# Optimization experiments

Measured on AMD Instinct MI355X. Metric: run time of the kernel, lower is better.

## Reference

```python
import jax, jax.numpy as jnp
import numpy as np

N_HEADS = 16
EPS = 1e-5  # torch nn.LayerNorm default


def layernorm(x, g, b):
    mu = x.mean(-1, keepdims=True)
    var = ((x - mu) ** 2).mean(-1, keepdims=True)
    return (x - mu) * jax.lax.rsqrt(var + EPS) * g + b


def setup_inputs() -> dict:
    V, D, Dff, L, S, B = 32000, 1024, 4096, 6, 2048, 1
    key = jax.random.key(0)
    ks = jax.random.split(key, 12)
    std = 0.02  # GPT-2 init
    nrm = lambda k, shp: jax.random.normal(k, shp, jnp.float32) * std
    return {
        "tokens": jax.random.randint(ks[0], (B, S), 0, V),
        "tok_emb": nrm(ks[1], (V, D)),          # tied with lm head
        "pos_emb": nrm(ks[2], (S, D)),
        "Wq": nrm(ks[3], (L, D, D)), "bq": jnp.zeros((L, D)),
        "Wk": nrm(ks[4], (L, D, D)), "bk": jnp.zeros((L, D)),
        "Wv": nrm(ks[5], (L, D, D)), "bv": jnp.zeros((L, D)),
        "Wo": nrm(ks[6], (L, D, D)), "bo": jnp.zeros((L, D)),
        "ln1_g": jnp.ones((L, D)), "ln1_b": jnp.zeros((L, D)),
        "ln2_g": jnp.ones((L, D)), "ln2_b": jnp.zeros((L, D)),
        "W1": nrm(ks[7], (L, D, Dff)), "b1": jnp.zeros((L, Dff)),
        "W2": nrm(ks[8], (L, Dff, D)), "b2": jnp.zeros((L, D)),
        "lnf_g": jnp.ones((D,)), "lnf_b": jnp.zeros((D,)),
    }


def reference(tokens, tok_emb, pos_emb, Wq, bq, Wk, bk, Wv, bv, Wo, bo,
              ln1_g, ln1_b, ln2_g, ln2_b, W1, b1, W2, b2, lnf_g, lnf_b):
    B, S = tokens.shape
    D = tok_emb.shape[1]
    dk = D // N_HEADS
    scale = 1.0 / np.sqrt(dk)

    x = tok_emb[tokens] + pos_emb[:S][None]           # (B,S,D); dropout p=0 -> identity
    causal = jnp.tril(jnp.ones((S, S), bool))

    def block(x, p):
        wq, bq_, wk, bk_, wv, bv_, wo, bo_, g1, b1_, g2, b2_, w1, bf1, w2, bf2 = p
        # --- attention sublayer (pre-norm) ---
        h = layernorm(x, g1, b1_)
        q = (h @ wq + bq_).reshape(B, S, N_HEADS, dk)
        k = (h @ wk + bk_).reshape(B, S, N_HEADS, dk)
        v = (h @ wv + bv_).reshape(B, S, N_HEADS, dk)
        scores = jnp.einsum('bqhd,bkhd->bhqk', q, k) * scale
        scores = jnp.where(causal, scores, -jnp.inf)   # masked_fill(mask==0, -inf)
        attn = jax.nn.softmax(scores, axis=-1)
        ctx = jnp.einsum('bhqk,bkhd->bqhd', attn, v).reshape(B, S, D)
        x = x + ctx @ wo + bo_
        # --- FFN sublayer (pre-norm) ---
        h = layernorm(x, g2, b2_)
        x = x + jax.nn.gelu(h @ w1 + bf1, approximate=False) @ w2 + bf2
        return x, None

    x, _ = jax.lax.scan(
        block, x,
        (Wq, bq, Wk, bk, Wv, bv, Wo, bo, ln1_g, ln1_b, ln2_g, ln2_b, W1, b1, W2, b2))
    x = layernorm(x, lnf_g, lnf_b)
    logits = x @ tok_emb.T                             # tied lm head (no bias)
    return logits
```

## Files before the change

kernel.cpp:

```cpp
#include <hip/hip_runtime.h>
#include <hip/hip_bf16.h>
#include <cstdint>
#include <cstddef>


typedef __attribute__((ext_vector_type(4))) float  f32x4;
typedef __attribute__((ext_vector_type(8))) __bf16 bf16x8;
typedef __attribute__((ext_vector_type(4))) __bf16 bf16x4;

#define S_LEN 2048
#define DMODEL 1024
#define DFF 4096
#define NLAYER 6
#define NHEAD 16
#define DK 64
#define VOCAB 32000
#define MN (S_LEN * DMODEL)

__device__ __forceinline__ void gload_lds16(const void* g, void* l) {
    __builtin_amdgcn_global_load_lds(
        (__attribute__((address_space(1))) void*)(void*)(g),
        (__attribute__((address_space(3))) void*)(l), 16, 0, 0);
}

__global__ __launch_bounds__(256) void transpose_cvt64(
    const float* __restrict__ in, __bf16* __restrict__ out,
    int K, int N, size_t in_lstride, size_t out_lstride) {
    __shared__ float tile[64][65];
    const float* inp = in + blockIdx.z * in_lstride;
    __bf16* outp = out + blockIdx.z * out_lstride;
    const int n0 = blockIdx.x * 64, k0 = blockIdx.y * 64;
    const int t = threadIdx.x;
    const int lc = t & 15, rr = t >> 4;
#pragma unroll
    for (int i = 0; i < 4; ++i) {
        float4 v = *(const float4*)&inp[(size_t)(k0 + rr + i * 16) * N + n0 + lc * 4];
        tile[rr + i * 16][lc * 4 + 0] = v.x;
        tile[rr + i * 16][lc * 4 + 1] = v.y;
        tile[rr + i * 16][lc * 4 + 2] = v.z;
        tile[rr + i * 16][lc * 4 + 3] = v.w;
    }
    __syncthreads();
    const int a = t & 7, b = t >> 3;
#pragma unroll
    for (int j = 0; j < 2; ++j) {
        const int n = b + j * 32;
        bf16x8 o;
#pragma unroll
        for (int e = 0; e < 8; ++e) o[e] = (__bf16)tile[a * 8 + e][n];
        *(bf16x8*)&outp[(size_t)(n0 + n) * K + k0 + a * 8] = o;
    }
}

__global__ __launch_bounds__(256) void cvt_bf16(
    const float* __restrict__ in, __bf16* __restrict__ out, long n4) {
    long i = (long)blockIdx.x * 256 + threadIdx.x;
    if (i >= n4) return;
    float4 v = ((const float4*)in)[i];
    bf16x4 o = {(__bf16)v.x, (__bf16)v.y, (__bf16)v.z, (__bf16)v.w};
    ((bf16x4*)out)[i] = o;
}

__global__ __launch_bounds__(256) void embed_kernel(
    const int* __restrict__ tokens, const float* __restrict__ te,
    const float* __restrict__ pe, float* __restrict__ x) {
    const int s = blockIdx.x, t = threadIdx.x;
    const int tok = tokens[s];
    float4 a = ((const float4*)(te + (size_t)tok * DMODEL))[t];
    float4 p = ((const float4*)(pe + (size_t)s * DMODEL))[t];
    float4 r = {a.x + p.x, a.y + p.y, a.z + p.z, a.w + p.w};
    ((float4*)(x + (size_t)s * DMODEL))[t] = r;
}

template <int NPART>
__global__ __launch_bounds__(256) void ln_kernel(
    float* __restrict__ x, const float* __restrict__ p,
    const float* __restrict__ g, const float* __restrict__ b,
    __bf16* __restrict__ out) {
    const int row = blockIdx.x, t = threadIdx.x;
    float4 v = ((const float4*)(x + (size_t)row * DMODEL))[t];
    if (NPART == 2) {
        float4 a0 = ((const float4*)(p + (size_t)row * DMODEL))[t];
        float4 a1 = ((const float4*)(p + MN + (size_t)row * DMODEL))[t];
        v.x += a0.x + a1.x;
        v.y += a0.y + a1.y;
        v.z += a0.z + a1.z;
        v.w += a0.w + a1.w;
        ((float4*)(x + (size_t)row * DMODEL))[t] = v;
    }
    float s  = v.x + v.y + v.z + v.w;
    float s2 = v.x * v.x + v.y * v.y + v.z * v.z + v.w * v.w;
#pragma unroll
    for (int off = 1; off < 64; off <<= 1) {
        s  += __shfl_xor(s, off);
        s2 += __shfl_xor(s2, off);
    }
    __shared__ float ss[4], ss2[4];
    const int wave = t >> 6;
    if ((t & 63) == 0) { ss[wave] = s; ss2[wave] = s2; }
    __syncthreads();
    s  = ss[0] + ss[1] + ss[2] + ss[3];
    s2 = ss2[0] + ss2[1] + ss2[2] + ss2[3];
    const float mu  = s * (1.0f / DMODEL);
    const float var = s2 * (1.0f / DMODEL) - mu * mu;
    const float rstd = rsqrtf(var + 1e-5f);
    float4 gg = ((const float4*)g)[t];
    float4 bb = ((const float4*)b)[t];
    __bf16* o = out + (size_t)row * DMODEL + t * 4;
    o[0] = (__bf16)((v.x - mu) * rstd * gg.x + bb.x);
    o[1] = (__bf16)((v.y - mu) * rstd * gg.y + bb.y);
    o[2] = (__bf16)((v.z - mu) * rstd * gg.z + bb.z);
    o[3] = (__bf16)((v.w - mu) * rstd * gg.w + bb.w);
}

template <int BM, int BN, int BK, int SPLITK, int MODE, int XCD>
__global__ __launch_bounds__(256) void gemm_tiled(
    const __bf16* __restrict__ A, const __bf16* __restrict__ BT,
    int M, int N, int K,
    const float* __restrict__ bias,
    float* __restrict__ fout,
    __bf16* __restrict__ bfout,
    __bf16* __restrict__ qb, __bf16* __restrict__ kb, __bf16* __restrict__ vb,
    const float* __restrict__ bq, const float* __restrict__ bk,
    const float* __restrict__ bv) {
    constexpr int SLOTS = BK / 8;
    constexpr int SH    = (BK == 64) ? 0 : 1;
    constexpr int RPC   = 2048 / BK;
    constexpr int ACH_A = BM / RPC;
    constexpr int ACH_B = BN / RPC;
    constexpr int LOADS = ACH_A + ACH_B;
    constexpr int MR = BM / 32;
    constexpr int NR = BN / 32;
    constexpr int KS = BK / 32;
    __shared__ alignas(16) __bf16 As[2][BM * BK];
    __shared__ alignas(16) __bf16 Bs[2][BN * BK];
    const int t = threadIdx.x;
    const int wave = t >> 6, lane = t & 63;
    const int wr = wave >> 1, wc = wave & 1;
    const int lg = lane >> 4, lr = lane & 15;

    int bx = blockIdx.x, by = blockIdx.y;
    if (XCD) {
        const int nwg = gridDim.x * gridDim.y;
        const int wgid = by * gridDim.x + bx;
        const int sw = (wgid & 7) * (nwg >> 3) + (wgid >> 3);
        bx = sw % gridDim.x;
        by = sw / gridDim.x;
    }
    const int row0 = bx * BM, col0 = by * BN;
    const int kz = (SPLITK > 1) ? blockIdx.z : 0;
    const int Ksl = K / SPLITK;

    f32x4 acc[MR][NR];
#pragma unroll
    for (int i = 0; i < MR; i++)
#pragma unroll
        for (int j = 0; j < NR; j++) acc[i][j] = f32x4{0.f, 0.f, 0.f, 0.f};

    const int srow = t / SLOTS;
    const int sks = ((t % SLOTS) ^ ((srow >> SH) & (SLOTS - 1))) * 8;
    const __bf16* Ab = A + (size_t)(row0 + srow) * K + kz * Ksl + sks;
    const __bf16* Bb = BT + (size_t)(col0 + srow) * K + kz * Ksl + sks;

    const int nt = Ksl / BK;
#pragma unroll
    for (int ch = 0; ch < ACH_A; ++ch)
        gload_lds16(Ab + (size_t)ch * RPC * K, &As[0][ch * 2048 + wave * 512]);
#pragma unroll
    for (int ch = 0; ch < ACH_B; ++ch)
        gload_lds16(Bb + (size_t)ch * RPC * K, &Bs[0][ch * 2048 + wave * 512]);

    int c = 0;
    for (int T = 0; T < nt; ++T) {
        if (T + 1 < nt) {
            const int k0 = (T + 1) * BK;
#pragma unroll
            for (int ch = 0; ch < ACH_A; ++ch)
                gload_lds16(Ab + (size_t)ch * RPC * K + k0,
                            &As[c ^ 1][ch * 2048 + wave * 512]);
#pragma unroll
            for (int ch = 0; ch < ACH_B; ++ch)
                gload_lds16(Bb + (size_t)ch * RPC * K + k0,
                            &Bs[c ^ 1][ch * 2048 + wave * 512]);
            if constexpr (LOADS == 3)
                asm volatile("s_waitcnt vmcnt(3)" ::: "memory");
            else if constexpr (LOADS == 4)
                asm volatile("s_waitcnt vmcnt(4)" ::: "memory");
            else if constexpr (LOADS == 6)
                asm volatile("s_waitcnt vmcnt(6)" ::: "memory");
            else
                asm volatile("s_waitcnt vmcnt(8)" ::: "memory");
        } else {
            asm volatile("s_waitcnt vmcnt(0)" ::: "memory");
        }
        __builtin_amdgcn_s_barrier();
        asm volatile("" ::: "memory");

        bf16x8 af[MR][KS], bfr[NR][KS];
#pragma unroll
        for (int i = 0; i < MR; i++)
#pragma unroll
            for (int ks = 0; ks < KS; ks++) {
                const int row = wr * (BM / 2) + i * 16 + lr;
                const int ph = ((ks * 4 + lg) ^ ((row >> SH) & (SLOTS - 1)));
                af[i][ks] = *(const bf16x8*)&As[c][row * BK + ph * 8];
            }
#pragma unroll
        for (int j = 0; j < NR; j++)
#pragma unroll
            for (int ks = 0; ks < KS; ks++) {
                const int n = wc * (BN / 2) + j * 16 + lr;
                const int ph = ((ks * 4 + lg) ^ ((n >> SH) & (SLOTS - 1)));
                bfr[j][ks] = *(const bf16x8*)&Bs[c][n * BK + ph * 8];
            }
        __builtin_amdgcn_s_setprio(1);
#pragma unroll
        for (int i = 0; i < MR; i++)
#pragma unroll
            for (int j = 0; j < NR; j++)
#pragma unroll
                for (int ks = 0; ks < KS; ks++)
                    acc[i][j] = __builtin_amdgcn_mfma_f32_16x16x32_bf16(
                        af[i][ks], bfr[j][ks], acc[i][j], 0, 0, 0);
        __builtin_amdgcn_s_setprio(0);
        asm volatile("" ::: "memory");
        __builtin_amdgcn_s_barrier();
        c ^= 1;
    }

#pragma unroll
    for (int i = 0; i < MR; i++) {
#pragma unroll
        for (int j = 0; j < NR; j++) {
#pragma unroll
            for (int r = 0; r < 4; r++) {
                const int row = row0 + wr * (BM / 2) + i * 16 + lg * 4 + r;
                const int col = col0 + wc * (BN / 2) + j * 16 + lr;
                float v = acc[i][j][r];
                if (MODE == 0) {
                    const int sec = col >> 10, cn = col & 1023;
                    const int head = cn >> 6, d = cn & 63;
                    if (sec == 0) {
                        v = (v + bq[cn]) * 0.18033688011112042f;
                        qb[((size_t)head * S_LEN + row) * DK + d] = (__bf16)v;
                    } else if (sec == 1) {
                        v = v + bk[cn];
                        kb[((size_t)head * S_LEN + row) * DK + d] = (__bf16)v;
                    } else {
                        v = v + bv[cn];
                        vb[((size_t)head * DK + d) * S_LEN + row] = (__bf16)v;
                    }
                } else if (MODE == 2) {
                    const float gg = v + bias[col];
                    const float cgl = 0.5f * gg * (1.0f + erff(gg * 0.70710678118654752f));
                    bfout[(size_t)row * N + col] = (__bf16)cgl;
                } else if (MODE == 6) {
                    const float vv = v + (kz == 0 ? bias[col] : 0.f);
                    __builtin_nontemporal_store(
                        vv, &fout[(size_t)kz * MN + (size_t)row * N + col]);
                } else {
                    __builtin_nontemporal_store(v, &fout[(size_t)row * N + col]);
                }
            }
        }
    }
}

__global__ __launch_bounds__(256) void attn_kernel(
    const __bf16* __restrict__ q, const __bf16* __restrict__ k,
    const __bf16* __restrict__ vt, __bf16* __restrict__ ctx) {
    const int xb = blockIdx.x, head = blockIdx.y;
    const int t = threadIdx.x;
    const int wave = t >> 6, lane = t & 63;
    const int lg = lane >> 4, lr = lane & 15;
    const int rg = (wave < 2) ? (2 * xb + wave) : (127 - 2 * xb - (3 - wave));
    const int rowbase = rg * 16;
    const int tend = rg >> 2;

    const __bf16* qh = q + (size_t)head * S_LEN * DK;
    const __bf16* kh = k + (size_t)head * S_LEN * DK;
    const __bf16* vh = vt + (size_t)head * DK * S_LEN;

    __shared__ alignas(16) __bf16 pls[4][16 * 72];
    __bf16* pw = pls[wave];

    bf16x8 qf0 = *(const bf16x8*)&qh[(size_t)(rowbase + lr) * DK + lg * 8];
    bf16x8 qf1 = *(const bf16x8*)&qh[(size_t)(rowbase + lr) * DK + 32 + lg * 8];

    f32x4 oacc[4];
#pragma unroll
    for (int j = 0; j < 4; j++) oacc[j] = f32x4{0.f, 0.f, 0.f, 0.f};
    float m[4], l[4];
#pragma unroll
    for (int r = 0; r < 4; r++) { m[r] = -__builtin_inff(); l[r] = 0.f; }

    for (int tt = 0; tt <= tend; ++tt) {
        const int kv0 = tt * 64;
        f32x4 sc[4];
        __builtin_amdgcn_s_setprio(1);
#pragma unroll
        for (int jn = 0; jn < 4; jn++) {
            bf16x8 kf0 = *(const bf16x8*)&kh[(size_t)(kv0 + jn * 16 + lr) * DK + lg * 8];
            bf16x8 kf1 = *(const bf16x8*)&kh[(size_t)(kv0 + jn * 16 + lr) * DK + 32 + lg * 8];
            sc[jn] = __builtin_amdgcn_mfma_f32_16x16x32_bf16(
                qf0, kf0, f32x4{0.f, 0.f, 0.f, 0.f}, 0, 0, 0);
            sc[jn] = __builtin_amdgcn_mfma_f32_16x16x32_bf16(qf1, kf1, sc[jn], 0, 0, 0);
        }
        __builtin_amdgcn_s_setprio(0);

        if (tt == tend) {
#pragma unroll
            for (int jn = 0; jn < 4; jn++)
#pragma unroll
                for (int r = 0; r < 4; r++) {
                    const int qrow = rowbase + lg * 4 + r;
                    if (kv0 + jn * 16 + lr > qrow) sc[jn][r] = -__builtin_inff();
                }
        }

        float mt[4];
#pragma unroll
        for (int r = 0; r < 4; r++)
            mt[r] = fmaxf(fmaxf(sc[0][r], sc[1][r]), fmaxf(sc[2][r], sc[3][r]));
#pragma unroll
        for (int off = 1; off < 16; off <<= 1)
#pragma unroll
            for (int r = 0; r < 4; r++) mt[r] = fmaxf(mt[r], __shfl_xor(mt[r], off));

        float alpha[4], psum[4];
#pragma unroll
        for (int r = 0; r < 4; r++) {
            const float mn = fmaxf(m[r], mt[r]);
            alpha[r] = exp2f(m[r] - mn);
            m[r] = mn;
#pragma unroll
            for (int jn = 0; jn < 4; jn++) sc[jn][r] = exp2f(sc[jn][r] - mn);
            psum[r] = (sc[0][r] + sc[1][r]) + (sc[2][r] + sc[3][r]);
        }
#pragma unroll
        for (int off = 1; off < 16; off <<= 1)
#pragma unroll
            for (int r = 0; r < 4; r++) psum[r] += __shfl_xor(psum[r], off);
#pragma unroll
        for (int r = 0; r < 4; r++) l[r] = l[r] * alpha[r] + psum[r];
#pragma unroll
        for (int j = 0; j < 4; j++)
#pragma unroll
            for (int r = 0; r < 4; r++) oacc[j][r] *= alpha[r];

#pragma unroll
        for (int r = 0; r < 4; r++)
#pragma unroll
            for (int jn = 0; jn < 4; jn++)
                pw[(lg * 4 + r) * 72 + jn * 16 + lr] = (__bf16)sc[jn][r];

        bf16x8 pf0 = *(const bf16x8*)&pw[lr * 72 + lg * 8];
        bf16x8 pf1 = *(const bf16x8*)&pw[lr * 72 + 32 + lg * 8];
        __builtin_amdgcn_s_setprio(1);
#pragma unroll
        for (int j = 0; j < 4; j++) {
            bf16x8 vf0 = *(const bf16x8*)&vh[(size_t)(j * 16 + lr) * S_LEN + kv0 + lg * 8];
            oacc[j] = __builtin_amdgcn_mfma_f32_16x16x32_bf16(pf0, vf0, oacc[j], 0, 0, 0);
            bf16x8 vf1 = *(const bf16x8*)&vh[(size_t)(j * 16 + lr) * S_LEN + kv0 + 32 + lg * 8];
            oacc[j] = __builtin_amdgcn_mfma_f32_16x16x32_bf16(pf1, vf1, oacc[j], 0, 0, 0);
        }
        __builtin_amdgcn_s_setprio(0);
    }

#pragma unroll
    for (int j = 0; j < 4; j++)
#pragma unroll
        for (int r = 0; r < 4; r++) {
            const int row = rowbase + lg * 4 + r;
            ctx[(size_t)row * DMODEL + head * DK + j * 16 + lr] =
                (__bf16)(oacc[j][r] / l[r]);
        }
}

extern "C" void kernel_launch(void* const* d_in, const int* in_sizes, int n_in,
                              void* d_out, int out_size, void* d_ws, size_t ws_size,
                              hipStream_t stream) {
    const int*   tokens  = (const int*)d_in[0];
    const float* tok_emb = (const float*)d_in[1];
    const float* pos_emb = (const float*)d_in[2];
    const float* Wq = (const float*)d_in[3];
    const float* bq = (const float*)d_in[4];
    const float* Wk = (const float*)d_in[5];
    const float* bk = (const float*)d_in[6];
    const float* Wv = (const float*)d_in[7];
    const float* bv = (const float*)d_in[8];
    const float* Wo = (const float*)d_in[9];
    const float* bo = (const float*)d_in[10];
    const float* ln1_g = (const float*)d_in[11];
    const float* ln1_b = (const float*)d_in[12];
    const float* ln2_g = (const float*)d_in[13];
    const float* ln2_b = (const float*)d_in[14];
    const float* W1 = (const float*)d_in[15];
    const float* b1 = (const float*)d_in[16];
    const float* W2 = (const float*)d_in[17];
    const float* b2 = (const float*)d_in[18];
    const float* lnf_g = (const float*)d_in[19];
    const float* lnf_b = (const float*)d_in[20];

    char* ws = (char*)d_ws;
    size_t off = 0;
    auto alloc = [&](size_t bytes) {
        char* p = ws + off;
        off = (off + bytes + 255) & ~(size_t)255;
        return p;
    };
    __bf16* wqkv_t = (__bf16*)alloc((size_t)NLAYER * 3072 * 1024 * 2);
    __bf16* wo_t   = (__bf16*)alloc((size_t)NLAYER * 1024 * 1024 * 2);
    __bf16* w1_t   = (__bf16*)alloc((size_t)NLAYER * 4096 * 1024 * 2);
    __bf16* w2_t   = (__bf16*)alloc((size_t)NLAYER * 1024 * 4096 * 2);
    __bf16* temb   = (__bf16*)alloc((size_t)VOCAB * DMODEL * 2);
    float*  x      = (float*)alloc((size_t)MN * 4);
    __bf16* h      = (__bf16*)alloc((size_t)MN * 2);
    __bf16* qbuf   = (__bf16*)alloc((size_t)MN * 2);
    __bf16* kbuf   = (__bf16*)alloc((size_t)MN * 2);
    __bf16* vbuf   = (__bf16*)alloc((size_t)MN * 2);
    __bf16* ctx    = (__bf16*)alloc((size_t)MN * 2);
    __bf16* ffn    = (__bf16*)alloc((size_t)S_LEN * DFF * 2);
    if (off > ws_size) return;

    float* pproj  = (float*)ffn;
    float* pffn2  = (float*)qbuf;

    const dim3 blk256(256);

    transpose_cvt64<<<dim3(16, 16, NLAYER), blk256, 0, stream>>>(
        Wq, wqkv_t + (size_t)0 * 1024 * 1024, 1024, 1024,
        (size_t)1024 * 1024, (size_t)3072 * 1024);
    transpose_cvt64<<<dim3(16, 16, NLAYER), blk256, 0, stream>>>(
        Wk, wqkv_t + (size_t)1 * 1024 * 1024, 1024, 1024,
        (size_t)1024 * 1024, (size_t)3072 * 1024);
    transpose_cvt64<<<dim3(16, 16, NLAYER), blk256, 0, stream>>>(
        Wv, wqkv_t + (size_t)2 * 1024 * 1024, 1024, 1024,
        (size_t)1024 * 1024, (size_t)3072 * 1024);
    transpose_cvt64<<<dim3(16, 16, NLAYER), blk256, 0, stream>>>(
        Wo, wo_t, 1024, 1024, (size_t)1024 * 1024, (size_t)1024 * 1024);
    transpose_cvt64<<<dim3(64, 16, NLAYER), blk256, 0, stream>>>(
        W1, w1_t, 1024, 4096, (size_t)1024 * 4096, (size_t)4096 * 1024);
    transpose_cvt64<<<dim3(16, 64, NLAYER), blk256, 0, stream>>>(
        W2, w2_t, 4096, 1024, (size_t)4096 * 1024, (size_t)1024 * 4096);
    cvt_bf16<<<dim3((VOCAB * DMODEL / 4 + 255) / 256), blk256, 0, stream>>>(
        tok_emb, temb, (long)VOCAB * DMODEL / 4);

    embed_kernel<<<dim3(S_LEN), blk256, 0, stream>>>(tokens, tok_emb, pos_emb, x);
    ln_kernel<0><<<dim3(S_LEN), blk256, 0, stream>>>(
        x, nullptr, ln1_g, ln1_b, h);

    for (int l = 0; l < NLAYER; ++l) {
        gemm_tiled<64, 128, 64, 1, 0, 0><<<dim3(32, 24), blk256, 0, stream>>>(
            h, wqkv_t + (size_t)l * 3072 * 1024, S_LEN, 3072, 1024,
            nullptr, nullptr, nullptr, qbuf, kbuf, vbuf,
            bq + l * 1024, bk + l * 1024, bv + l * 1024);
        attn_kernel<<<dim3(32, NHEAD), blk256, 0, stream>>>(
            qbuf, kbuf, vbuf, ctx);
        gemm_tiled<64, 128, 64, 2, 6, 0><<<dim3(32, 8, 2), blk256, 0, stream>>>(
            ctx, wo_t + (size_t)l * 1024 * 1024, S_LEN, 1024, 1024,
            bo + l * 1024, pproj, nullptr, nullptr, nullptr, nullptr,
            nullptr, nullptr, nullptr);
        ln_kernel<2><<<dim3(S_LEN), blk256, 0, stream>>>(
            x, pproj, ln2_g + l * 1024, ln2_b + l * 1024, h);
        gemm_tiled<128, 128, 64, 1, 2, 0><<<dim3(16, 32), blk256, 0, stream>>>(
            h, w1_t + (size_t)l * 4096 * 1024, S_LEN, 4096, 1024,
            b1 + l * 4096, nullptr, ffn, nullptr, nullptr, nullptr,
            nullptr, nullptr, nullptr);
        gemm_tiled<64, 128, 64, 2, 6, 0><<<dim3(32, 8, 2), blk256, 0, stream>>>(
            ffn, w2_t + (size_t)l * 1024 * 4096, S_LEN, 1024, 4096,
            b2 + l * 1024, pffn2, nullptr, nullptr, nullptr, nullptr,
            nullptr, nullptr, nullptr);
        if (l + 1 < NLAYER) {
            ln_kernel<2><<<dim3(S_LEN), blk256, 0, stream>>>(
                x, pffn2, ln1_g + (l + 1) * 1024, ln1_b + (l + 1) * 1024, h);
        }
    }

    ln_kernel<2><<<dim3(S_LEN), blk256, 0, stream>>>(x, pffn2, lnf_g, lnf_b, h);
    gemm_tiled<128, 256, 32, 1, 3, 1><<<dim3(16, 125), blk256, 0, stream>>>(
        h, temb, S_LEN, VOCAB, 1024,
        nullptr, (float*)d_out, nullptr, nullptr, nullptr, nullptr,
        nullptr, nullptr, nullptr);
}
```

Before: 1.717 ms.

## Widen attention KV tile, merge QKVO transposes, fuse embed into LayerNorm, retile QKV GEMM

The attention kernel now processes 128 keys per iteration instead of 64, which halves the loop trips and softmax reductions but needs more registers and a larger LDS P buffer. The four Q/K/V/O weight transposes become one launch, and the embedding lookup is folded into the first LayerNorm kernel, removing launches and one round trip of x through memory. The QKV projection GEMM switches to 128-row tiles, which gives fewer, larger blocks. The wider attention tile also makes causal-diagonal handling coarser, so some fully masked work is wasted.

```diff
diff --git a/kernel.cpp b/kernel.cpp
--- a/kernel.cpp
+++ b/kernel.cpp
@@ -23,14 +23,10 @@
         (__attribute__((address_space(3))) void*)(l), 16, 0, 0);
 }
 
-__global__ __launch_bounds__(256) void transpose_cvt64(
-    const float* __restrict__ in, __bf16* __restrict__ out,
-    int K, int N, size_t in_lstride, size_t out_lstride) {
+__device__ __forceinline__ void tr64_body(
+    const float* __restrict__ inp, __bf16* __restrict__ outp,
+    int K, int N, int n0, int k0, int t) {
     __shared__ float tile[64][65];
-    const float* inp = in + blockIdx.z * in_lstride;
-    __bf16* outp = out + blockIdx.z * out_lstride;
-    const int n0 = blockIdx.x * 64, k0 = blockIdx.y * 64;
-    const int t = threadIdx.x;
     const int lc = t & 15, rr = t >> 4;
 #pragma unroll
     for (int i = 0; i < 4; ++i) {
@@ -50,6 +46,27 @@
         for (int e = 0; e < 8; ++e) o[e] = (__bf16)tile[a * 8 + e][n];
         *(bf16x8*)&outp[(size_t)(n0 + n) * K + k0 + a * 8] = o;
     }
+}
+
+__global__ __launch_bounds__(256) void transpose_cvt64(
+    const float* __restrict__ in, __bf16* __restrict__ out,
+    int K, int N, size_t in_lstride, size_t out_lstride) {
+    tr64_body(in + blockIdx.z * in_lstride, out + blockIdx.z * out_lstride,
+              K, N, blockIdx.x * 64, blockIdx.y * 64, threadIdx.x);
+}
+
+__global__ __launch_bounds__(256) void transpose_qkvo(
+    const float* __restrict__ Wq, const float* __restrict__ Wk,
+    const float* __restrict__ Wv, const float* __restrict__ Wo,
+    __bf16* __restrict__ wqkv_t, __bf16* __restrict__ wo_t) {
+    const int z = blockIdx.z, mat = z & 3, l = z >> 2;
+    const float* src =
+        (mat == 0 ? Wq : mat == 1 ? Wk : mat == 2 ? Wv : Wo) +
+        (size_t)l * 1024 * 1024;
+    __bf16* dst = (mat < 3)
+        ? wqkv_t + (size_t)l * 3072 * 1024 + (size_t)mat * 1024 * 1024
+        : wo_t + (size_t)l * 1024 * 1024;
+    tr64_body(src, dst, 1024, 1024, blockIdx.x * 64, blockIdx.y * 64, threadIdx.x);
 }
 
 __global__ __launch_bounds__(256) void cvt_bf16(
@@ -61,24 +78,24 @@
     ((bf16x4*)out)[i] = o;
 }
 
-__global__ __launch_bounds__(256) void embed_kernel(
-    const int* __restrict__ tokens, const float* __restrict__ te,
-    const float* __restrict__ pe, float* __restrict__ x) {
-    const int s = blockIdx.x, t = threadIdx.x;
-    const int tok = tokens[s];
-    float4 a = ((const float4*)(te + (size_t)tok * DMODEL))[t];
-    float4 p = ((const float4*)(pe + (size_t)s * DMODEL))[t];
-    float4 r = {a.x + p.x, a.y + p.y, a.z + p.z, a.w + p.w};
-    ((float4*)(x + (size_t)s * DMODEL))[t] = r;
-}
-
-template <int NPART>
+template <int NPART, int EMBED>
 __global__ __launch_bounds__(256) void ln_kernel(
     float* __restrict__ x, const float* __restrict__ p,
     const float* __restrict__ g, const float* __restrict__ b,
-    __bf16* __restrict__ out) {
+    __bf16* __restrict__ out,
+    const int* __restrict__ tokens, const float* __restrict__ te,
+    const float* __restrict__ pe) {
     const int row = blockIdx.x, t = threadIdx.x;
-    float4 v = ((const float4*)(x + (size_t)row * DMODEL))[t];
+    float4 v;
+    if (EMBED) {
+        const int tok = tokens[row];
+        float4 a = ((const float4*)(te + (size_t)tok * DMODEL))[t];
+        float4 q = ((const float4*)(pe + (size_t)row * DMODEL))[t];
+        v = float4{a.x + q.x, a.y + q.y, a.z + q.z, a.w + q.w};
+        ((float4*)(x + (size_t)row * DMODEL))[t] = v;
+    } else {
+        v = ((const float4*)(x + (size_t)row * DMODEL))[t];
+    }
     if (NPART == 2) {
         float4 a0 = ((const float4*)(p + (size_t)row * DMODEL))[t];
         float4 a1 = ((const float4*)(p + MN + (size_t)row * DMODEL))[t];
@@ -275,13 +292,13 @@
     const int lg = lane >> 4, lr = lane & 15;
     const int rg = (wave < 2) ? (2 * xb + wave) : (127 - 2 * xb - (3 - wave));
     const int rowbase = rg * 16;
-    const int tend = rg >> 2;
+    const int tend = rg >> 3;
 
     const __bf16* qh = q + (size_t)head * S_LEN * DK;
     const __bf16* kh = k + (size_t)head * S_LEN * DK;
     const __bf16* vh = vt + (size_t)head * DK * S_LEN;
 
-    __shared__ alignas(16) __bf16 pls[4][16 * 72];
+    __shared__ alignas(16) __bf16 pls[4][16 * 136];
     __bf16* pw = pls[wave];
 
     bf16x8 qf0 = *(const bf16x8*)&qh[(size_t)(rowbase + lr) * DK + lg * 8];
@@ -295,11 +312,11 @@
     for (int r = 0; r < 4; r++) { m[r] = -__builtin_inff(); l[r] = 0.f; }
 
     for (int tt = 0; tt <= tend; ++tt) {
-        const int kv0 = tt * 64;
-        f32x4 sc[4];
+        const int kv0 = tt * 128;
+        f32x4 sc[8];
         __builtin_amdgcn_s_setprio(1);
 #pragma unroll
-        for (int jn = 0; jn < 4; jn++) {
+        for (int jn = 0; jn < 8; jn++) {
             bf16x8 kf0 = *(const bf16x8*)&kh[(size_t)(kv0 + jn * 16 + lr) * DK + lg * 8];
             bf16x8 kf1 = *(const bf16x8*)&kh[(size_t)(kv0 + jn * 16 + lr) * DK + 32 + lg * 8];
             sc[jn] = __builtin_amdgcn_mfma_f32_16x16x32_bf16(
@@ -310,7 +327,7 @@
 
         if (tt == tend) {
 #pragma unroll
-            for (int jn = 0; jn < 4; jn++)
+            for (int jn = 0; jn < 8; jn++)
 #pragma unroll
                 for (int r = 0; r < 4; r++) {
                     const int qrow = rowbase + lg * 4 + r;
@@ -320,8 +337,11 @@
 
         float mt[4];
 #pragma unroll
-        for (int r = 0; r < 4; r++)
-            mt[r] = fmaxf(fmaxf(sc[0][r], sc[1][r]), fmaxf(sc[2][r], sc[3][r]));
+        for (int r = 0; r < 4; r++) {
+            float a0 = fmaxf(fmaxf(sc[0][r], sc[1][r]), fmaxf(sc[2][r], sc[3][r]));
+            float a1 = fmaxf(fmaxf(sc[4][r], sc[5][r]), fmaxf(sc[6][r], sc[7][r]));
+            mt[r] = fmaxf(a0, a1);
+        }
 #pragma unroll
         for (int off = 1; off < 16; off <<= 1)
 #pragma unroll
@@ -334,8 +354,9 @@
             alpha[r] = exp2f(m[r] - mn);
             m[r] = mn;
 #pragma unroll
-            for (int jn = 0; jn < 4; jn++) sc[jn][r] = exp2f(sc[jn][r] - mn);
-            psum[r] = (sc[0][r] + sc[1][r]) + (sc[2][r] + sc[3][r]);
+            for (int jn = 0; jn < 8; jn++) sc[jn][r] = exp2f(sc[jn][r] - mn);
+            psum[r] = ((sc[0][r] + sc[1][r]) + (sc[2][r] + sc[3][r])) +
+                      ((sc[4][r] + sc[5][r]) + (sc[6][r] + sc[7][r]));
         }
 #pragma unroll
         for (int off = 1; off < 16; off <<= 1)
@@ -351,18 +372,23 @@
 #pragma unroll
         for (int r = 0; r < 4; r++)
 #pragma unroll
-            for (int jn = 0; jn < 4; jn++)
-                pw[(lg * 4 + r) * 72 + jn * 16 + lr] = (__bf16)sc[jn][r];
-
-        bf16x8 pf0 = *(const bf16x8*)&pw[lr * 72 + lg * 8];
-        bf16x8 pf1 = *(const bf16x8*)&pw[lr * 72 + 32 + lg * 8];
+            for (int jn = 0; jn < 8; jn++)
+                pw[(lg * 4 + r) * 136 + jn * 16 + lr] = (__bf16)sc[jn][r];
+
+        bf16x8 pf[4];
+#pragma unroll
+        for (int h = 0; h < 4; h++)
+            pf[h] = *(const bf16x8*)&pw[lr * 136 + h * 32 + lg * 8];
         __builtin_amdgcn_s_setprio(1);
 #pragma unroll
         for (int j = 0; j < 4; j++) {
-            bf16x8 vf0 = *(const bf16x8*)&vh[(size_t)(j * 16 + lr) * S_LEN + kv0 + lg * 8];
-            oacc[j] = __builtin_amdgcn_mfma_f32_16x16x32_bf16(pf0, vf0, oacc[j], 0, 0, 0);
-            bf16x8 vf1 = *(const bf16x8*)&vh[(size_t)(j * 16 + lr) * S_LEN + kv0 + 32 + lg * 8];
-            oacc[j] = __builtin_amdgcn_mfma_f32_16x16x32_bf16(pf1, vf1, oacc[j], 0, 0, 0);
+#pragma unroll
+            for (int h = 0; h < 4; h++) {
+                bf16x8 vf = *(const bf16x8*)
+                    &vh[(size_t)(j * 16 + lr) * S_LEN + kv0 + h * 32 + lg * 8];
+                oacc[j] = __builtin_amdgcn_mfma_f32_16x16x32_bf16(
+                    pf[h], vf, oacc[j], 0, 0, 0);
+            }
         }
         __builtin_amdgcn_s_setprio(0);
     }
@@ -428,17 +454,8 @@
 
     const dim3 blk256(256);
 
-    transpose_cvt64<<<dim3(16, 16, NLAYER), blk256, 0, stream>>>(
-        Wq, wqkv_t + (size_t)0 * 1024 * 1024, 1024, 1024,
-        (size_t)1024 * 1024, (size_t)3072 * 1024);
-    transpose_cvt64<<<dim3(16, 16, NLAYER), blk256, 0, stream>>>(
-        Wk, wqkv_t + (size_t)1 * 1024 * 1024, 1024, 1024,
-        (size_t)1024 * 1024, (size_t)3072 * 1024);
-    transpose_cvt64<<<dim3(16, 16, NLAYER), blk256, 0, stream>>>(
-        Wv, wqkv_t + (size_t)2 * 1024 * 1024, 1024, 1024,
-        (size_t)1024 * 1024, (size_t)3072 * 1024);
-    transpose_cvt64<<<dim3(16, 16, NLAYER), blk256, 0, stream>>>(
-        Wo, wo_t, 1024, 1024, (size_t)1024 * 1024, (size_t)1024 * 1024);
+    transpose_qkvo<<<dim3(16, 16, 4 * NLAYER), blk256, 0, stream>>>(
+        Wq, Wk, Wv, Wo, wqkv_t, wo_t);
     transpose_cvt64<<<dim3(64, 16, NLAYER), blk256, 0, stream>>>(
         W1, w1_t, 1024, 4096, (size_t)1024 * 4096, (size_t)4096 * 1024);
     transpose_cvt64<<<dim3(16, 64, NLAYER), blk256, 0, stream>>>(
@@ -446,12 +463,11 @@
     cvt_bf16<<<dim3((VOCAB * DMODEL / 4 + 255) / 256), blk256, 0, stream>>>(
         tok_emb, temb, (long)VOCAB * DMODEL / 4);
 
-    embed_kernel<<<dim3(S_LEN), blk256, 0, stream>>>(tokens, tok_emb, pos_emb, x);
-    ln_kernel<0><<<dim3(S_LEN), blk256, 0, stream>>>(
-        x, nullptr, ln1_g, ln1_b, h);
+    ln_kernel<0, 1><<<dim3(S_LEN), blk256, 0, stream>>>(
+        x, nullptr, ln1_g, ln1_b, h, tokens, tok_emb, pos_emb);
 
     for (int l = 0; l < NLAYER; ++l) {
-        gemm_tiled<64, 128, 64, 1, 0, 0><<<dim3(32, 24), blk256, 0, stream>>>(
+        gemm_tiled<128, 128, 64, 1, 0, 0><<<dim3(16, 24), blk256, 0, stream>>>(
             h, wqkv_t + (size_t)l * 3072 * 1024, S_LEN, 3072, 1024,
             nullptr, nullptr, nullptr, qbuf, kbuf, vbuf,
             bq + l * 1024, bk + l * 1024, bv + l * 1024);
@@ -461,8 +477,9 @@
             ctx, wo_t + (size_t)l * 1024 * 1024, S_LEN, 1024, 1024,
             bo + l * 1024, pproj, nullptr, nullptr, nullptr, nullptr,
             nullptr, nullptr, nullptr);
-        ln_kernel<2><<<dim3(S_LEN), blk256, 0, stream>>>(
-            x, pproj, ln2_g + l * 1024, ln2_b + l * 1024, h);
+        ln_kernel<2, 0><<<dim3(S_LEN), blk256, 0, stream>>>(
+            x, pproj, ln2_g + l * 1024, ln2_b + l * 1024, h,
+            nullptr, nullptr, nullptr);
         gemm_tiled<128, 128, 64, 1, 2, 0><<<dim3(16, 32), blk256, 0, stream>>>(
             h, w1_t + (size_t)l * 4096 * 1024, S_LEN, 4096, 1024,
             b1 + l * 4096, nullptr, ffn, nullptr, nullptr, nullptr,
@@ -472,12 +489,14 @@
             b2 + l * 1024, pffn2, nullptr, nullptr, nullptr, nullptr,
             nullptr, nullptr, nullptr);
         if (l + 1 < NLAYER) {
-            ln_kernel<2><<<dim3(S_LEN), blk256, 0, stream>>>(
-                x, pffn2, ln1_g + (l + 1) * 1024, ln1_b + (l + 1) * 1024, h);
-        }
-    }
-
-    ln_kernel<2><<<dim3(S_LEN), blk256, 0, stream>>>(x, pffn2, lnf_g, lnf_b, h);
+            ln_kernel<2, 0><<<dim3(S_LEN), blk256, 0, stream>>>(
+                x, pffn2, ln1_g + (l + 1) * 1024, ln1_b + (l + 1) * 1024, h,
+                nullptr, nullptr, nullptr);
+        }
+    }
+
+    ln_kernel<2, 0><<<dim3(S_LEN), blk256, 0, stream>>>(
+        x, pffn2, lnf_g, lnf_b, h, nullptr, nullptr, nullptr);
     gemm_tiled<128, 256, 32, 1, 3, 1><<<dim3(16, 125), blk256, 0, stream>>>(
         h, temb, S_LEN, VOCAB, 1024,
         nullptr, (float*)d_out, nullptr, nullptr, nullptr, nullptr,
```

New measurement: 1.598 ms. -7.0%, faster.
